# Kernel tuning notes

Hardware: AMD Instinct MI355X
Metric: run time of the kernel (lower is better)

## Reference

```python
import jax, jax.numpy as jnp
import numpy as np

B, T, S_ENC, D = 2, 1024, 1024, 2048
NQ, NKV, H = 16, 8, 256
EPS = 1e-6
CAP = 50.0
SCALE = 0.0625  # query_pre_attn_scalar = head_dim**-0.5
BASE = 10000
K_MASK = -2.3819763e+38


def rms_norm(x, scale, eps=EPS):
    var = jnp.mean(jnp.square(x), axis=-1, keepdims=True)
    return x * jax.lax.rsqrt(var + eps) * (1.0 + scale)


def apply_rope(x, positions, base=BASE):
    # x: [B, L, N, H], positions: [B, L] float. rope_proportion=1.0 -> full head.
    head_dim = x.shape[-1]
    timescale = base ** (2.0 / head_dim * jnp.arange(head_dim // 2, dtype=jnp.float32))
    sinusoid = positions[..., None] / timescale  # [B, L, H/2]
    sinusoid = sinusoid[..., None, :]            # [B, L, 1, H/2]
    sin, cos = jnp.sin(sinusoid), jnp.cos(sinusoid)
    x1, x2 = jnp.split(x, 2, axis=-1)
    return jnp.concatenate([x1 * cos - x2 * sin, x2 * cos + x1 * sin], axis=-1).astype(x.dtype)


def setup_inputs() -> dict:
    key = jax.random.key(0)
    ks = jax.random.split(key, 6)
    hidden_states = jax.random.normal(ks[0], (B, T, D), jnp.float32)
    encoder_hidden_states = jax.random.normal(ks[1], (B, S_ENC, D), jnp.float32)
    position_ids = jnp.broadcast_to(jnp.arange(T, dtype=jnp.int32), (B, T))
    causal = jnp.tril(jnp.ones((T, T), bool))
    merged = jnp.concatenate([causal, jnp.ones((T, S_ENC), bool)], axis=-1)
    merged_attention_mask = jnp.broadcast_to(merged[None, None], (B, 1, T, T + S_ENC))
    q_w = jax.random.normal(ks[2], (NQ, D, H), jnp.float32) * 0.02
    k_w = jax.random.normal(ks[3], (NKV, D, H), jnp.float32) * 0.02
    v_w = jax.random.normal(ks[4], (NKV, D, H), jnp.float32) * 0.02
    o_w = jax.random.normal(ks[5], (NQ, H, D), jnp.float32) * 0.02
    q_scale = jnp.zeros((H,), jnp.float32)
    k_scale = jnp.zeros((H,), jnp.float32)
    return {
        'hidden_states': hidden_states,
        'encoder_hidden_states': encoder_hidden_states,
        'position_ids': position_ids,
        'merged_attention_mask': merged_attention_mask,
        'q_w': q_w, 'k_w': k_w, 'v_w': v_w, 'o_w': o_w,
        'q_scale': q_scale, 'k_scale': k_scale,
    }


def reference(hidden_states, encoder_hidden_states, position_ids, merged_attention_mask,
              q_w, k_w, v_w, o_w, q_scale, k_scale):
    # Fused QKV projections
    q = jnp.einsum('BTD,NDH->BTNH', hidden_states, q_w)
    self_k = jnp.einsum('BTD,NDH->BTNH', hidden_states, k_w)
    self_v = jnp.einsum('BTD,NDH->BTNH', hidden_states, v_w)
    # QK RMSNorm
    q = rms_norm(q, q_scale)
    self_k = rms_norm(self_k, k_scale)
    # RoPE on decoder-side q/k only
    pos = position_ids.astype(jnp.float32)
    q = apply_rope(q, pos)
    self_k = apply_rope(self_k, pos)
    # Cross KV (no RoPE, k-norm applied)
    cross_k = rms_norm(jnp.einsum('BTD,NDH->BTNH', encoder_hidden_states, k_w), k_scale)
    cross_v = jnp.einsum('BTD,NDH->BTNH', encoder_hidden_states, v_w)
    # Merge KV: [B, T+S_enc, NKV, H]
    k = jnp.concatenate([self_k, cross_k], axis=1)
    v = jnp.concatenate([self_v, cross_v], axis=1)
    q = q * SCALE
    # GQA: group query heads over kv heads
    G = NQ // NKV
    qg = q.reshape(B, T, NKV, G, H)
    logits = jnp.einsum('BTKGH,BSKH->BKGTS', qg, k)
    # Logit soft-cap
    logits = CAP * jnp.tanh(logits / CAP)
    mask = merged_attention_mask[:, 0][:, None, None]  # [B,1,1,T,S_comb]
    logits = jnp.where(mask, logits, K_MASK)
    probs = jax.nn.softmax(logits, axis=-1)
    out = jnp.einsum('BKGTS,BSKH->BTKGH', probs, v).reshape(B, T, NQ, H)
    return jnp.einsum('BTNH,NHD->BTD', out, o_w)
```

## Files before the change

kernel.cpp:

```cpp
#include <hip/hip_runtime.h>
#include <hip/hip_bf16.h>
#include <stdint.h>

typedef __hip_bfloat16 bf16;
typedef __attribute__((ext_vector_type(8))) short bv8;
typedef __attribute__((ext_vector_type(4))) float f32x4;


__device__ __forceinline__ f32x4 mfma16(bv8 a, bv8 b, f32x4 c) {
  return __builtin_amdgcn_mfma_f32_16x16x32_bf16(a, b, c, 0, 0, 0);
}

__device__ __forceinline__ void gload16(const void* g, void* lds) {
  __builtin_amdgcn_global_load_lds((const __attribute__((address_space(1))) void*)g,
                                   (__attribute__((address_space(3))) void*)lds, 16, 0, 0);
}

__device__ __forceinline__ void storeC(float* p, float v) { *p = v; }
__device__ __forceinline__ void storeC(bf16* p, float v) { *p = __float2bfloat16(v); }

__global__ void cast2_f32_bf16(const float* __restrict__ a, const float* __restrict__ b,
                               bf16* __restrict__ da, bf16* __restrict__ db, int n4each) {
  int i = blockIdx.x * blockDim.x + threadIdx.x;
  const float* s;
  bf16* d;
  if (i < n4each) { s = a; d = da; }
  else            { s = b; d = db; i -= n4each; }
  float4 v = reinterpret_cast<const float4*>(s)[i];
  bf16 t[4] = {__float2bfloat16(v.x), __float2bfloat16(v.y),
               __float2bfloat16(v.z), __float2bfloat16(v.w)};
  reinterpret_cast<uint64_t*>(d)[i] = *reinterpret_cast<uint64_t*>(t);
}

__global__ void transpose_cast_qkv(const float* __restrict__ q_w, const float* __restrict__ k_w,
                                   const float* __restrict__ v_w, bf16* __restrict__ dst) {
  __shared__ float tile[32][33];
  const int z = blockIdx.z;
  const float* s = (z < 16) ? q_w + (size_t)z * 524288
                 : (z < 24) ? k_w + (size_t)(z - 16) * 524288
                            : v_w + (size_t)(z - 24) * 524288;
  bf16* d = dst + (size_t)z * 524288;
  const int R = 2048, C = 256;
  const int c0 = blockIdx.x * 32, r0 = blockIdx.y * 32;
  const int x = threadIdx.x, y = threadIdx.y;
#pragma unroll
  for (int i = 0; i < 32; i += 8)
    tile[y + i][x] = s[(size_t)(r0 + y + i) * C + c0 + x];
  __syncthreads();
#pragma unroll
  for (int i = 0; i < 32; i += 8)
    d[(size_t)(c0 + y + i) * R + r0 + x] = __float2bfloat16(tile[x][y + i]);
}

__global__ void transpose_cast(const float* __restrict__ src, bf16* __restrict__ dst,
                               int R, int C) {
  __shared__ float tile[32][33];
  const float* s = src;
  bf16* d = dst;
  const int c0 = blockIdx.x * 32, r0 = blockIdx.y * 32;
  const int x = threadIdx.x, y = threadIdx.y;
#pragma unroll
  for (int i = 0; i < 32; i += 8)
    tile[y + i][x] = s[(size_t)(r0 + y + i) * C + c0 + x];
  __syncthreads();
#pragma unroll
  for (int i = 0; i < 32; i += 8)
    d[(size_t)(c0 + y + i) * R + r0 + x] = __float2bfloat16(tile[x][y + i]);
}

__global__ void transpose_v2(const bf16* __restrict__ vself, const bf16* __restrict__ vcross,
                             bf16* __restrict__ dst) {
  __shared__ bf16 tile[32][33];
  const int z = blockIdx.z;
  const int zz = z & 15, b = zz >> 3, kvh = zz & 7;
  const bool cross = z >= 16;
  const bf16* srcb = cross ? vcross : vself;
  const int src_ld = cross ? 4096 : 8192;
  const int t0 = cross ? 1024 : 0;
  const bf16* s = srcb + (size_t)(b * 1024) * src_ld + kvh * 256;
  bf16* d = dst + (size_t)(zz * 256) * 2048 + t0;
  const int h0 = blockIdx.x * 32, tt0 = blockIdx.y * 32;
  const int x = threadIdx.x, y = threadIdx.y;
#pragma unroll
  for (int i = 0; i < 32; i += 8)
    tile[y + i][x] = s[(size_t)(tt0 + y + i) * src_ld + h0 + x];
  __syncthreads();
#pragma unroll
  for (int i = 0; i < 32; i += 8)
    d[(size_t)(h0 + y + i) * 2048 + tt0 + x] = tile[x][y + i];
}

template <typename CT>
__device__ __forceinline__ void gemm_body(const bf16* __restrict__ A, const bf16* __restrict__ Bt,
                                          CT* __restrict__ C, int N, int K,
                                          int m0, int n0, int kbase, int ksteps) {
  __shared__ __align__(16) bf16 As[128 * 32];
  __shared__ __align__(16) bf16 Bs[128 * 32];
  const int tid = threadIdx.x;
  const int w = tid >> 6, l = tid & 63;
  const int wr = w >> 1, wc = w & 1;
  const int l15 = l & 15, lhi = l >> 4;
  const bf16* ag = A + (size_t)(m0 + (tid >> 2)) * K + kbase + (tid & 3) * 8;
  const bf16* bg = Bt + (size_t)(n0 + (tid >> 2)) * K + kbase + (tid & 3) * 8;
  bf16* asw = As + w * 512;
  bf16* bsw = Bs + w * 512;
  f32x4 acc[4][4] = {};
  for (int k0 = 0; k0 < ksteps; k0 += 32) {
    gload16(ag + k0, asw);
    gload16(ag + (size_t)64 * K + k0, asw + 2048);
    gload16(bg + k0, bsw);
    gload16(bg + (size_t)64 * K + k0, bsw + 2048);
    asm volatile("s_waitcnt vmcnt(0)" ::: "memory");
    __syncthreads();
    bv8 af[4], bfv[4];
#pragma unroll
    for (int m = 0; m < 4; ++m)
      af[m] = *reinterpret_cast<const bv8*>(As + (wr * 64 + m * 16 + l15) * 32 + lhi * 8);
#pragma unroll
    for (int n = 0; n < 4; ++n)
      bfv[n] = *reinterpret_cast<const bv8*>(Bs + (wc * 64 + n * 16 + l15) * 32 + lhi * 8);
#pragma unroll
    for (int m = 0; m < 4; ++m)
#pragma unroll
      for (int n = 0; n < 4; ++n)
        acc[m][n] = mfma16(af[m], bfv[n], acc[m][n]);
    __syncthreads();
  }
  const int r0 = m0 + wr * 64 + lhi * 4;
  const int c0 = n0 + wc * 64 + l15;
#pragma unroll
  for (int m = 0; m < 4; ++m)
#pragma unroll
    for (int n = 0; n < 4; ++n) {
      f32x4 v = acc[m][n];
#pragma unroll
      for (int j = 0; j < 4; ++j)
        storeC(&C[(size_t)(r0 + m * 16 + j) * N + c0 + n * 16], v[j]);
    }
}

__launch_bounds__(256)
__global__ void gemm_proj(const bf16* __restrict__ hid, const bf16* __restrict__ enc,
                          const bf16* __restrict__ wqkvt, bf16* __restrict__ cself,
                          bf16* __restrict__ ccross) {
  const int bx = blockIdx.x;
  const bool cross = bx >= 64;
  const bf16* A = cross ? enc : hid;
  const bf16* Bt = cross ? wqkvt + 8388608 : wqkvt;
  bf16* C = cross ? ccross : cself;
  const int N = cross ? 4096 : 8192;
  const int n0 = (cross ? bx - 64 : bx) * 128;
  gemm_body<bf16>(A, Bt, C, N, 2048, blockIdx.y * 128, n0, 0, 2048);
}

__launch_bounds__(256)
__global__ void gemm_osplit(const bf16* __restrict__ A, const bf16* __restrict__ Bt,
                            float* __restrict__ out, float* __restrict__ p1) {
  float* C = blockIdx.z ? p1 : out;
  gemm_body<float>(A, Bt, C, 2048, 4096, blockIdx.y * 128, blockIdx.x * 128,
                   blockIdx.z * 2048, 2048);
}

__global__ void add_inplace(float* __restrict__ out, const float* __restrict__ p1, int n4) {
  int i = blockIdx.x * blockDim.x + threadIdx.x;
  if (i >= n4) return;
  float4 a = reinterpret_cast<float4*>(out)[i];
  float4 b = reinterpret_cast<const float4*>(p1)[i];
  a.x += b.x; a.y += b.y; a.z += b.z; a.w += b.w;
  reinterpret_cast<float4*>(out)[i] = a;
}

template <bool ROPE>
__launch_bounds__(256)
__global__ void norm_finalize(const bf16* __restrict__ src, int src_ld, int src_col0,
                              const float* __restrict__ scale,
                              const int* __restrict__ pos_ids,
                              bf16* __restrict__ dst, int nheads, int dst_S, int dst_t0,
                              float mul) {
  const int gid = blockIdx.x * 4 + (threadIdx.x >> 6);
  const int l = threadIdx.x & 63;
  const int token = gid / nheads;
  const int n = gid - token * nheads;
  const int b = token >> 10;
  const int t = token & 1023;
  const size_t soff = (size_t)token * src_ld + src_col0 + n * 256 + l * 4;
  bf16 xb[4];
  *reinterpret_cast<uint64_t*>(xb) = *reinterpret_cast<const uint64_t*>(src + soff);
  float x[4];
#pragma unroll
  for (int c = 0; c < 4; ++c) x[c] = __bfloat162float(xb[c]);
  float ss = x[0] * x[0] + x[1] * x[1] + x[2] * x[2] + x[3] * x[3];
#pragma unroll
  for (int d = 1; d < 64; d <<= 1) ss += __shfl_xor(ss, d);
  const float r = rsqrtf(ss * (1.0f / 256.0f) + 1e-6f);
  float v[4];
#pragma unroll
  for (int c = 0; c < 4; ++c) v[c] = x[c] * r * (1.0f + scale[l * 4 + c]);
  if (ROPE) {
    const float pos = (float)pos_ids[token];
    float o[4];
#pragma unroll
    for (int c = 0; c < 4; ++c) {
      const int j = (l & 31) * 4 + c;
      const float inv_ts = exp2f(-(float)j * 0.10381025296523007f);
      const float arg = pos * inv_ts;
      const float sj = sinf(arg), cj = cosf(arg);
      const float partner = __shfl_xor(v[c], 32);
      o[c] = (l < 32) ? (v[c] * cj - partner * sj) : (v[c] * cj + partner * sj);
    }
#pragma unroll
    for (int c = 0; c < 4; ++c) v[c] = o[c];
  }
  bf16 ob[4];
#pragma unroll
  for (int c = 0; c < 4; ++c) ob[c] = __float2bfloat16(v[c] * mul);
  const size_t doff = ((size_t)((b * nheads + n) * dst_S + dst_t0 + t)) * 256 + l * 4;
  *reinterpret_cast<uint64_t*>(dst + doff) = *reinterpret_cast<uint64_t*>(ob);
}

__launch_bounds__(512, 2)
__global__ void attn_kernel(const bf16* __restrict__ qb, const bf16* __restrict__ kb,
                            const bf16* __restrict__ vt, bf16* __restrict__ attn_out) {
  __shared__ __align__(16) bf16 Ks[2][64 * 256];
  __shared__ __align__(16) bf16 Vs[2][256 * 64];
  __shared__ __align__(16) bf16 pbuf[8][16 * 72];
  const int lin = blockIdx.x + 16 * blockIdx.y;
  const int kvc = (lin & 7) | (((lin >> 7) & 1) << 3);
  const int qt  = (lin >> 3) & 15;
  const int b = kvc >> 3, kvh = kvc & 7;
  const int tid = threadIdx.x, w = tid >> 6, l = tid & 63;
  const int wq = w & 3, g = w >> 2;
  const int n = kvh * 2 + g;
  const int l15 = l & 15, lhi = l >> 4;
  const int xr = (l15 & 7) << 4;

  const bf16* kbase = kb + (size_t)(b * 8 + kvh) * 2048 * 256;
  const bf16* vbase = vt + (size_t)(b * 8 + kvh) * 256 * 2048;

  const bf16* ksrc[4];
  const bf16* vsrc[4];
#pragma unroll
  for (int i = 0; i < 4; ++i) {
    const int r0 = (w * 4 + i) * 2 + (l >> 5);
    const int cbs = ((l & 31) * 16) ^ ((r0 & 7) << 4);
    ksrc[i] = kbase + r0 * 256 + (cbs >> 1);
    const int h0 = (w * 4 + i) * 8 + (l >> 3);
    const int cbv = ((l & 7) * 16) ^ ((h0 & 7) << 4);
    vsrc[i] = vbase + (size_t)h0 * 2048 + (cbv >> 1);
  }

  const bf16* qptr = qb + ((size_t)(b * 16 + n) * 1024 + qt * 64 + wq * 16 + l15) * 256 + lhi * 8;
  bv8 qf[8];
#pragma unroll
  for (int f = 0; f < 8; ++f) qf[f] = *reinterpret_cast<const bv8*>(qptr + f * 32);

  f32x4 oacc[16] = {};
  float rs[4] = {0.f, 0.f, 0.f, 0.f};

  const int nt = qt + 17;

#pragma unroll
  for (int i = 0; i < 4; ++i) gload16(ksrc[i], &Ks[0][(w * 4 + i) * 512]);
#pragma unroll
  for (int i = 0; i < 4; ++i) gload16(vsrc[i], &Vs[0][(w * 4 + i) * 512]);
  asm volatile("s_waitcnt vmcnt(0)" ::: "memory");
  __syncthreads();

  for (int it = 0; it < nt; ++it) {
    const int cur = it & 1;
    if (it + 1 < nt) {
      const int itn = it + 1;
      const int s1 = (itn <= qt) ? itn * 64 : 1024 + (itn - qt - 1) * 64;
#pragma unroll
      for (int i = 0; i < 4; ++i)
        gload16(ksrc[i] + (size_t)s1 * 256, &Ks[cur ^ 1][(w * 4 + i) * 512]);
#pragma unroll
      for (int i = 0; i < 4; ++i)
        gload16(vsrc[i] + s1, &Vs[cur ^ 1][(w * 4 + i) * 512]);
    }
    f32x4 lacc[4] = {};
    __builtin_amdgcn_s_setprio(1);
#pragma unroll
    for (int sub = 0; sub < 4; ++sub) {
      const int rbase = (sub * 16 + l15) * 256;
#pragma unroll
      for (int f = 0; f < 8; ++f) {
        const int off = rbase + (((f * 64 + lhi * 16) ^ xr) >> 1);
        bv8 kf = *reinterpret_cast<const bv8*>(&Ks[cur][off]);
        lacc[sub] = mfma16(qf[f], kf, lacc[sub]);
      }
    }
    __builtin_amdgcn_s_setprio(0);
    const bool diag = (it == qt);
#pragma unroll
    for (int sub = 0; sub < 4; ++sub) {
#pragma unroll
      for (int j = 0; j < 4; ++j) {
        const float raw = lacc[sub][j];
        const float e2 = __expf(raw * 0.04f);
        const bool ok = !diag || (sub * 16 + l15 <= wq * 16 + lhi * 4 + j);
        const float p = ok ? __expf(50.f - __fdividef(100.f, e2 + 1.f)) : 0.f;
        rs[j] += p;
        pbuf[w][(lhi * 4 + j) * 72 + sub * 16 + l15] = __float2bfloat16(p);
      }
    }
    asm volatile("s_waitcnt lgkmcnt(0)" ::: "memory");
    __builtin_amdgcn_sched_barrier(0);
    __builtin_amdgcn_s_setprio(1);
#pragma unroll
    for (int ks = 0; ks < 2; ++ks) {
      bv8 pa = *reinterpret_cast<const bv8*>(&pbuf[w][l15 * 72 + ks * 32 + lhi * 8]);
#pragma unroll
      for (int ht = 0; ht < 16; ++ht) {
        const int off = (ht * 16 + l15) * 64 + (((ks * 64 + lhi * 16) ^ xr) >> 1);
        bv8 vf = *reinterpret_cast<const bv8*>(&Vs[cur][off]);
        oacc[ht] = mfma16(pa, vf, oacc[ht]);
      }
    }
    __builtin_amdgcn_s_setprio(0);
    asm volatile("s_waitcnt vmcnt(0)" ::: "memory");
    __syncthreads();
  }
  float invr[4];
#pragma unroll
  for (int j = 0; j < 4; ++j) {
    float s = rs[j];
    s += __shfl_xor(s, 1);
    s += __shfl_xor(s, 2);
    s += __shfl_xor(s, 4);
    s += __shfl_xor(s, 8);
    invr[j] = 1.0f / s;
  }
  bf16* op = attn_out + ((size_t)(b * 1024 + qt * 64 + wq * 16 + lhi * 4) * 4096) + n * 256 + l15;
#pragma unroll
  for (int ht = 0; ht < 16; ++ht)
#pragma unroll
    for (int j = 0; j < 4; ++j)
      op[(size_t)j * 4096 + ht * 16] = __float2bfloat16(oacc[ht][j] * invr[j]);
}

extern "C" void kernel_launch(void* const* d_in, const int* in_sizes, int n_in,
                              void* d_out, int out_size, void* d_ws, size_t ws_size,
                              hipStream_t stream) {
  (void)in_sizes; (void)n_in; (void)out_size; (void)ws_size;
  const float* hidden = (const float*)d_in[0];
  const float* enc    = (const float*)d_in[1];
  const int*   pos    = (const int*)d_in[2];
  const float* q_w = (const float*)d_in[4];
  const float* k_w = (const float*)d_in[5];
  const float* v_w = (const float*)d_in[6];
  const float* o_w = (const float*)d_in[7];
  const float* q_s = (const float*)d_in[8];
  const float* k_s = (const float*)d_in[9];
  float* out = (float*)d_out;

  char* base = (char*)d_ws;
  bf16* hid_b  = (bf16*)(base + 0);
  bf16* enc_b  = (bf16*)(base + 8388608);
  bf16* qb     = (bf16*)(base + 0);
  bf16* wqkvt  = (bf16*)(base + 16777216);
  bf16* kbuf   = (bf16*)(base + 16777216);
  bf16* vtb    = (bf16*)(base + 33554432);
  bf16* owt    = (bf16*)(base + 50331648);
  bf16* cself  = (bf16*)(base + 67108864);
  bf16* attn_b = (bf16*)(base + 67108864);
  float* p1    = (float*)(base + 83886080);
  bf16* ccross = (bf16*)(base + 100663296);

  dim3 tb32(32, 8);
  cast2_f32_bf16<<<8192, 256, 0, stream>>>(hidden, enc, hid_b, enc_b, 1048576);
  transpose_cast_qkv<<<dim3(8, 64, 32), tb32, 0, stream>>>(q_w, k_w, v_w, wqkvt);
  transpose_cast<<<dim3(64, 128, 1), tb32, 0, stream>>>(o_w, owt, 4096, 2048);
  gemm_proj<<<dim3(96, 16), 256, 0, stream>>>(hid_b, enc_b, wqkvt, cself, ccross);
  norm_finalize<true><<<8192, 256, 0, stream>>>(cself, 8192, 0, q_s, pos, qb, 16, 1024, 0, 0.0625f);
  norm_finalize<true><<<4096, 256, 0, stream>>>(cself, 8192, 4096, k_s, pos, kbuf, 8, 2048, 0, 1.0f);
  norm_finalize<false><<<4096, 256, 0, stream>>>(ccross, 4096, 0, k_s, nullptr, kbuf, 8, 2048, 1024, 1.0f);
  transpose_v2<<<dim3(8, 32, 32), tb32, 0, stream>>>(cself + 6144, ccross + 2048, vtb);
  attn_kernel<<<dim3(16, 16), 512, 0, stream>>>(qb, kbuf, vtb, attn_b);
  gemm_osplit<<<dim3(16, 16, 2), 256, 0, stream>>>(attn_b, owt, out, p1);
  add_inplace<<<4096, 256, 0, stream>>>(out, p1, 1048576);
}
```

Measured before the change: 376.4 us.

## Repartition attention warps into 2x2 QK and head-dim split PV tiles

Each warp now computes a 32x32 block of the logits (two query subtiles by two key subtiles) instead of 16 queries by all 64 keys. In the PV product each warp covers all 64 queries but only a quarter of the head dimension. Probabilities are shared through a per-group LDS buffer, and row sums are combined across warps via shared memory. This lets each K and V fragment read from LDS feed several MFMAs, cutting LDS traffic per MFMA. The cost is an extra block-wide barrier per iteration, a final reduction step, and twice the Q fragments held in registers.

```diff
diff --git a/kernel.cpp b/kernel.cpp
--- a/kernel.cpp
+++ b/kernel.cpp
@@ -223,13 +223,14 @@
                             const bf16* __restrict__ vt, bf16* __restrict__ attn_out) {
   __shared__ __align__(16) bf16 Ks[2][64 * 256];
   __shared__ __align__(16) bf16 Vs[2][256 * 64];
-  __shared__ __align__(16) bf16 pbuf[8][16 * 72];
+  __shared__ __align__(16) bf16 pbuf[2][64 * 72];
+  __shared__ float rsb[2][2][2][2][4][4];
   const int lin = blockIdx.x + 16 * blockIdx.y;
   const int kvc = (lin & 7) | (((lin >> 7) & 1) << 3);
   const int qt  = (lin >> 3) & 15;
   const int b = kvc >> 3, kvh = kvc & 7;
   const int tid = threadIdx.x, w = tid >> 6, l = tid & 63;
-  const int wq = w & 3, g = w >> 2;
+  const int g = w >> 2, qsp = (w >> 1) & 1, sh = w & 1, hq = w & 3;
   const int n = kvh * 2 + g;
   const int l15 = l & 15, lhi = l >> 4;
   const int xr = (l15 & 7) << 4;
@@ -249,13 +250,17 @@
     vsrc[i] = vbase + (size_t)h0 * 2048 + (cbv >> 1);
   }
 
-  const bf16* qptr = qb + ((size_t)(b * 16 + n) * 1024 + qt * 64 + wq * 16 + l15) * 256 + lhi * 8;
-  bv8 qf[8];
-#pragma unroll
-  for (int f = 0; f < 8; ++f) qf[f] = *reinterpret_cast<const bv8*>(qptr + f * 32);
-
-  f32x4 oacc[16] = {};
-  float rs[4] = {0.f, 0.f, 0.f, 0.f};
+  bv8 qf[2][8];
+#pragma unroll
+  for (int qs2 = 0; qs2 < 2; ++qs2) {
+    const bf16* qp = qb + ((size_t)(b * 16 + n) * 1024 + qt * 64 +
+                           (qsp * 2 + qs2) * 16 + l15) * 256 + lhi * 8;
+#pragma unroll
+    for (int f = 0; f < 8; ++f) qf[qs2][f] = *reinterpret_cast<const bv8*>(qp + f * 32);
+  }
+
+  f32x4 oacc[4][4] = {};
+  float rs[2][4] = {};
 
   const int nt = qt + 17;
 
@@ -278,65 +283,84 @@
       for (int i = 0; i < 4; ++i)
         gload16(vsrc[i] + s1, &Vs[cur ^ 1][(w * 4 + i) * 512]);
     }
-    f32x4 lacc[4] = {};
+    f32x4 lacc[2][2] = {};
     __builtin_amdgcn_s_setprio(1);
 #pragma unroll
-    for (int sub = 0; sub < 4; ++sub) {
-      const int rbase = (sub * 16 + l15) * 256;
+    for (int ss2 = 0; ss2 < 2; ++ss2) {
+      const int rbase = ((sh * 2 + ss2) * 16 + l15) * 256;
 #pragma unroll
       for (int f = 0; f < 8; ++f) {
         const int off = rbase + (((f * 64 + lhi * 16) ^ xr) >> 1);
         bv8 kf = *reinterpret_cast<const bv8*>(&Ks[cur][off]);
-        lacc[sub] = mfma16(qf[f], kf, lacc[sub]);
+        lacc[0][ss2] = mfma16(qf[0][f], kf, lacc[0][ss2]);
+        lacc[1][ss2] = mfma16(qf[1][f], kf, lacc[1][ss2]);
       }
     }
     __builtin_amdgcn_s_setprio(0);
     const bool diag = (it == qt);
 #pragma unroll
-    for (int sub = 0; sub < 4; ++sub) {
-#pragma unroll
-      for (int j = 0; j < 4; ++j) {
-        const float raw = lacc[sub][j];
-        const float e2 = __expf(raw * 0.04f);
-        const bool ok = !diag || (sub * 16 + l15 <= wq * 16 + lhi * 4 + j);
-        const float p = ok ? __expf(50.f - __fdividef(100.f, e2 + 1.f)) : 0.f;
-        rs[j] += p;
-        pbuf[w][(lhi * 4 + j) * 72 + sub * 16 + l15] = __float2bfloat16(p);
-      }
-    }
-    asm volatile("s_waitcnt lgkmcnt(0)" ::: "memory");
-    __builtin_amdgcn_sched_barrier(0);
+    for (int qs2 = 0; qs2 < 2; ++qs2)
+#pragma unroll
+      for (int ss2 = 0; ss2 < 2; ++ss2)
+#pragma unroll
+        for (int j = 0; j < 4; ++j) {
+          const float raw = lacc[qs2][ss2][j];
+          const float e2 = __expf(raw * 0.04f);
+          const bool ok = !diag ||
+              ((sh * 2 + ss2) * 16 + l15 <= (qsp * 2 + qs2) * 16 + lhi * 4 + j);
+          const float p = ok ? __expf(50.f - __fdividef(100.f, e2 + 1.f)) : 0.f;
+          rs[qs2][j] += p;
+          pbuf[g][((qsp * 2 + qs2) * 16 + lhi * 4 + j) * 72 + (sh * 2 + ss2) * 16 + l15] =
+              __float2bfloat16(p);
+        }
+    __syncthreads();
     __builtin_amdgcn_s_setprio(1);
 #pragma unroll
     for (int ks = 0; ks < 2; ++ks) {
-      bv8 pa = *reinterpret_cast<const bv8*>(&pbuf[w][l15 * 72 + ks * 32 + lhi * 8]);
-#pragma unroll
-      for (int ht = 0; ht < 16; ++ht) {
-        const int off = (ht * 16 + l15) * 64 + (((ks * 64 + lhi * 16) ^ xr) >> 1);
+      bv8 pa[4];
+#pragma unroll
+      for (int qs = 0; qs < 4; ++qs)
+        pa[qs] = *reinterpret_cast<const bv8*>(&pbuf[g][(qs * 16 + l15) * 72 + ks * 32 + lhi * 8]);
+#pragma unroll
+      for (int i = 0; i < 4; ++i) {
+        const int off = ((hq * 4 + i) * 16 + l15) * 64 + (((ks * 64 + lhi * 16) ^ xr) >> 1);
         bv8 vf = *reinterpret_cast<const bv8*>(&Vs[cur][off]);
-        oacc[ht] = mfma16(pa, vf, oacc[ht]);
+#pragma unroll
+        for (int qs = 0; qs < 4; ++qs) oacc[qs][i] = mfma16(pa[qs], vf, oacc[qs][i]);
       }
     }
     __builtin_amdgcn_s_setprio(0);
     asm volatile("s_waitcnt vmcnt(0)" ::: "memory");
     __syncthreads();
   }
-  float invr[4];
-#pragma unroll
-  for (int j = 0; j < 4; ++j) {
-    float s = rs[j];
-    s += __shfl_xor(s, 1);
-    s += __shfl_xor(s, 2);
-    s += __shfl_xor(s, 4);
-    s += __shfl_xor(s, 8);
-    invr[j] = 1.0f / s;
-  }
-  bf16* op = attn_out + ((size_t)(b * 1024 + qt * 64 + wq * 16 + lhi * 4) * 4096) + n * 256 + l15;
-#pragma unroll
-  for (int ht = 0; ht < 16; ++ht)
+#pragma unroll
+  for (int qs2 = 0; qs2 < 2; ++qs2)
+#pragma unroll
+    for (int j = 0; j < 4; ++j) {
+      float s = rs[qs2][j];
+      s += __shfl_xor(s, 1);
+      s += __shfl_xor(s, 2);
+      s += __shfl_xor(s, 4);
+      s += __shfl_xor(s, 8);
+      if (l15 == 0) rsb[g][qsp][sh][qs2][j][lhi] = s;
+    }
+  __syncthreads();
+  float invr[4][4];
+#pragma unroll
+  for (int qs = 0; qs < 4; ++qs)
 #pragma unroll
     for (int j = 0; j < 4; ++j)
-      op[(size_t)j * 4096 + ht * 16] = __float2bfloat16(oacc[ht][j] * invr[j]);
+      invr[qs][j] = 1.0f / (rsb[g][qs >> 1][0][qs & 1][j][lhi] +
+                            rsb[g][qs >> 1][1][qs & 1][j][lhi]);
+  bf16* op = attn_out + ((size_t)(b * 1024 + qt * 64 + lhi * 4) * 4096) + n * 256 + l15;
+#pragma unroll
+  for (int qs = 0; qs < 4; ++qs)
+#pragma unroll
+    for (int i = 0; i < 4; ++i)
+#pragma unroll
+      for (int j = 0; j < 4; ++j)
+        op[(size_t)(qs * 16 + j) * 4096 + (hq * 4 + i) * 16] =
+            __float2bfloat16(oacc[qs][i][j] * invr[qs][j]);
 }
 
 extern "C" void kernel_launch(void* const* d_in, const int* in_sizes, int n_in,
```

Measured after the change: 370.0 us. No clear change (-1.7%).

## Halve attention query/key tiles and split score and PV work across warps

Applied to the files above, without the earlier changes.

The attention kernel now uses 32-row query tiles and 32-key KV tiles, which doubles the grid to 512 blocks and shrinks LDS use so up to four blocks can fit per CU. Each warp now computes one 16x16 score sub-tile and one quarter of the head dimension for PV. The probability tile is shared between warps through LDS, which needs an extra block-wide barrier every iteration. Row sums are combined across warps through a small LDS buffer at the end. The intent is more parallelism and occupancy for the causal-imbalanced workload, at the cost of more syncs and less data reuse per block. The exp calls are also switched to exp2f with pre-scaled constants.

```diff
diff --git a/kernel.cpp b/kernel.cpp
--- a/kernel.cpp
+++ b/kernel.cpp
@@ -218,18 +218,19 @@
   *reinterpret_cast<uint64_t*>(dst + doff) = *reinterpret_cast<uint64_t*>(ob);
 }
 
-__launch_bounds__(512, 2)
+__launch_bounds__(512, 4)
 __global__ void attn_kernel(const bf16* __restrict__ qb, const bf16* __restrict__ kb,
                             const bf16* __restrict__ vt, bf16* __restrict__ attn_out) {
-  __shared__ __align__(16) bf16 Ks[2][64 * 256];
-  __shared__ __align__(16) bf16 Vs[2][256 * 64];
-  __shared__ __align__(16) bf16 pbuf[8][16 * 72];
-  const int lin = blockIdx.x + 16 * blockIdx.y;
-  const int kvc = (lin & 7) | (((lin >> 7) & 1) << 3);
-  const int qt  = (lin >> 3) & 15;
+  __shared__ __align__(16) bf16 Ks[2][32 * 256];
+  __shared__ __align__(16) bf16 Vs[2][256 * 32];
+  __shared__ __align__(16) bf16 pbuf[2][32 * 36];
+  __shared__ float rsb[2][2][2][4][4];
+  const int lin = blockIdx.x + 32 * blockIdx.y;
+  const int kvc = (lin & 7) | (((lin >> 8) & 1) << 3);
+  const int qt  = (lin >> 3) & 31;
   const int b = kvc >> 3, kvh = kvc & 7;
   const int tid = threadIdx.x, w = tid >> 6, l = tid & 63;
-  const int wq = w & 3, g = w >> 2;
+  const int g = w >> 2, qs = (w >> 1) & 1, sh = w & 1, hq = w & 3;
   const int n = kvh * 2 + g;
   const int l15 = l & 15, lhi = l >> 4;
   const int xr = (l15 & 7) << 4;
@@ -237,32 +238,32 @@
   const bf16* kbase = kb + (size_t)(b * 8 + kvh) * 2048 * 256;
   const bf16* vbase = vt + (size_t)(b * 8 + kvh) * 256 * 2048;
 
-  const bf16* ksrc[4];
-  const bf16* vsrc[4];
-#pragma unroll
-  for (int i = 0; i < 4; ++i) {
-    const int r0 = (w * 4 + i) * 2 + (l >> 5);
-    const int cbs = ((l & 31) * 16) ^ ((r0 & 7) << 4);
-    ksrc[i] = kbase + r0 * 256 + (cbs >> 1);
-    const int h0 = (w * 4 + i) * 8 + (l >> 3);
-    const int cbv = ((l & 7) * 16) ^ ((h0 & 7) << 4);
-    vsrc[i] = vbase + (size_t)h0 * 2048 + (cbv >> 1);
-  }
-
-  const bf16* qptr = qb + ((size_t)(b * 16 + n) * 1024 + qt * 64 + wq * 16 + l15) * 256 + lhi * 8;
+  const int kcol = (((tid & 31) * 16) ^ (((tid >> 5) & 7) << 4)) >> 1;
+  const bf16* ksrc0 = kbase + (size_t)(tid >> 5) * 256 + kcol;
+  const bf16* ksrc1 = kbase + (size_t)(16 + (tid >> 5)) * 256 + kcol;
+  const int vcol = (((tid & 3) * 16) ^ (((tid >> 2) & 3) << 4)) >> 1;
+  const bf16* vsrc0 = vbase + (size_t)(tid >> 2) * 2048 + vcol;
+  const bf16* vsrc1 = vbase + (size_t)(128 + (tid >> 2)) * 2048 + vcol;
+
+#define STAGE_KV(bb, s0)                                         \
+  do {                                                           \
+    gload16(ksrc0 + (size_t)(s0) * 256, &Ks[bb][w * 512]);       \
+    gload16(ksrc1 + (size_t)(s0) * 256, &Ks[bb][4096 + w * 512]);\
+    gload16(vsrc0 + (s0), &Vs[bb][w * 512]);                     \
+    gload16(vsrc1 + (s0), &Vs[bb][4096 + w * 512]);              \
+  } while (0)
+
+  const bf16* qp = qb + ((size_t)(b * 16 + n) * 1024 + qt * 32 + qs * 16 + l15) * 256 + lhi * 8;
   bv8 qf[8];
 #pragma unroll
-  for (int f = 0; f < 8; ++f) qf[f] = *reinterpret_cast<const bv8*>(qptr + f * 32);
-
-  f32x4 oacc[16] = {};
-  float rs[4] = {0.f, 0.f, 0.f, 0.f};
-
-  const int nt = qt + 17;
-
-#pragma unroll
-  for (int i = 0; i < 4; ++i) gload16(ksrc[i], &Ks[0][(w * 4 + i) * 512]);
-#pragma unroll
-  for (int i = 0; i < 4; ++i) gload16(vsrc[i], &Vs[0][(w * 4 + i) * 512]);
+  for (int f = 0; f < 8; ++f) qf[f] = *reinterpret_cast<const bv8*>(qp + f * 32);
+
+  f32x4 oacc[2][4] = {};
+  float rs[4] = {};
+
+  const int nt = qt + 33;
+
+  STAGE_KV(0, 0);
   asm volatile("s_waitcnt vmcnt(0)" ::: "memory");
   __syncthreads();
 
@@ -270,58 +271,49 @@
     const int cur = it & 1;
     if (it + 1 < nt) {
       const int itn = it + 1;
-      const int s1 = (itn <= qt) ? itn * 64 : 1024 + (itn - qt - 1) * 64;
-#pragma unroll
-      for (int i = 0; i < 4; ++i)
-        gload16(ksrc[i] + (size_t)s1 * 256, &Ks[cur ^ 1][(w * 4 + i) * 512]);
-#pragma unroll
-      for (int i = 0; i < 4; ++i)
-        gload16(vsrc[i] + s1, &Vs[cur ^ 1][(w * 4 + i) * 512]);
-    }
-    f32x4 lacc[4] = {};
+      const int s1 = (itn <= qt) ? itn * 32 : 1024 + (itn - qt - 1) * 32;
+      STAGE_KV(cur ^ 1, s1);
+    }
+    f32x4 lacc = {};
+    const int krow = (sh * 16 + l15) * 256;
     __builtin_amdgcn_s_setprio(1);
 #pragma unroll
-    for (int sub = 0; sub < 4; ++sub) {
-      const int rbase = (sub * 16 + l15) * 256;
-#pragma unroll
-      for (int f = 0; f < 8; ++f) {
-        const int off = rbase + (((f * 64 + lhi * 16) ^ xr) >> 1);
-        bv8 kf = *reinterpret_cast<const bv8*>(&Ks[cur][off]);
-        lacc[sub] = mfma16(qf[f], kf, lacc[sub]);
-      }
+    for (int f = 0; f < 8; ++f) {
+      const int off = krow + (((f * 64 + lhi * 16) ^ xr) >> 1);
+      bv8 kf = *reinterpret_cast<const bv8*>(&Ks[cur][off]);
+      lacc = mfma16(qf[f], kf, lacc);
     }
     __builtin_amdgcn_s_setprio(0);
     const bool diag = (it == qt);
 #pragma unroll
-    for (int sub = 0; sub < 4; ++sub) {
-#pragma unroll
-      for (int j = 0; j < 4; ++j) {
-        const float raw = lacc[sub][j];
-        const float e2 = __expf(raw * 0.04f);
-        const bool ok = !diag || (sub * 16 + l15 <= wq * 16 + lhi * 4 + j);
-        const float p = ok ? __expf(50.f - __fdividef(100.f, e2 + 1.f)) : 0.f;
-        rs[j] += p;
-        pbuf[w][(lhi * 4 + j) * 72 + sub * 16 + l15] = __float2bfloat16(p);
-      }
-    }
-    asm volatile("s_waitcnt lgkmcnt(0)" ::: "memory");
-    __builtin_amdgcn_sched_barrier(0);
+    for (int j = 0; j < 4; ++j) {
+      const float raw = lacc[j];
+      const float e2 = exp2f(raw * 0.057707801635559464f);
+      const int trow = qs * 16 + lhi * 4 + j;
+      const bool ok = !diag || (sh * 16 + l15 <= trow);
+      const float p =
+          ok ? exp2f(72.13475204444817f - __fdividef(144.26950408889634f, e2 + 1.f)) : 0.f;
+      rs[j] += p;
+      pbuf[g][trow * 36 + sh * 16 + l15] = __float2bfloat16(p);
+    }
+    __syncthreads();
     __builtin_amdgcn_s_setprio(1);
-#pragma unroll
-    for (int ks = 0; ks < 2; ++ks) {
-      bv8 pa = *reinterpret_cast<const bv8*>(&pbuf[w][l15 * 72 + ks * 32 + lhi * 8]);
-#pragma unroll
-      for (int ht = 0; ht < 16; ++ht) {
-        const int off = (ht * 16 + l15) * 64 + (((ks * 64 + lhi * 16) ^ xr) >> 1);
-        bv8 vf = *reinterpret_cast<const bv8*>(&Vs[cur][off]);
-        oacc[ht] = mfma16(pa, vf, oacc[ht]);
-      }
+    bv8 pa[2];
+#pragma unroll
+    for (int q = 0; q < 2; ++q)
+      pa[q] = *reinterpret_cast<const bv8*>(&pbuf[g][(q * 16 + l15) * 36 + lhi * 8]);
+#pragma unroll
+    for (int i = 0; i < 4; ++i) {
+      const int off = ((hq * 4 + i) * 16 + l15) * 32 + ((lhi * 8) ^ ((l15 & 3) << 3));
+      bv8 vf = *reinterpret_cast<const bv8*>(&Vs[cur][off]);
+      oacc[0][i] = mfma16(pa[0], vf, oacc[0][i]);
+      oacc[1][i] = mfma16(pa[1], vf, oacc[1][i]);
     }
     __builtin_amdgcn_s_setprio(0);
     asm volatile("s_waitcnt vmcnt(0)" ::: "memory");
     __syncthreads();
   }
-  float invr[4];
+#undef STAGE_KV
 #pragma unroll
   for (int j = 0; j < 4; ++j) {
     float s = rs[j];
@@ -329,14 +321,24 @@
     s += __shfl_xor(s, 2);
     s += __shfl_xor(s, 4);
     s += __shfl_xor(s, 8);
-    invr[j] = 1.0f / s;
+    if (l15 == 0) rsb[g][qs][sh][j][lhi] = s;
   }
-  bf16* op = attn_out + ((size_t)(b * 1024 + qt * 64 + wq * 16 + lhi * 4) * 4096) + n * 256 + l15;
-#pragma unroll
-  for (int ht = 0; ht < 16; ++ht)
+  __syncthreads();
+  float invr[2][4];
+#pragma unroll
+  for (int q = 0; q < 2; ++q)
 #pragma unroll
     for (int j = 0; j < 4; ++j)
-      op[(size_t)j * 4096 + ht * 16] = __float2bfloat16(oacc[ht][j] * invr[j]);
+      invr[q][j] = 1.0f / (rsb[g][q][0][j][lhi] + rsb[g][q][1][j][lhi]);
+  bf16* op = attn_out + ((size_t)(b * 1024 + qt * 32 + lhi * 4) * 4096) + n * 256 + l15;
+#pragma unroll
+  for (int q = 0; q < 2; ++q)
+#pragma unroll
+    for (int i = 0; i < 4; ++i)
+#pragma unroll
+      for (int j = 0; j < 4; ++j)
+        op[(size_t)(q * 16 + j) * 4096 + (hq * 4 + i) * 16] =
+            __float2bfloat16(oacc[q][i][j] * invr[q][j]);
 }
 
 extern "C" void kernel_launch(void* const* d_in, const int* in_sizes, int n_in,
@@ -376,7 +378,7 @@
   norm_finalize<true><<<4096, 256, 0, stream>>>(cself, 8192, 4096, k_s, pos, kbuf, 8, 2048, 0, 1.0f);
   norm_finalize<false><<<4096, 256, 0, stream>>>(ccross, 4096, 0, k_s, nullptr, kbuf, 8, 2048, 1024, 1.0f);
   transpose_v2<<<dim3(8, 32, 32), tb32, 0, stream>>>(cself + 6144, ccross + 2048, vtb);
-  attn_kernel<<<dim3(16, 16), 512, 0, stream>>>(qb, kbuf, vtb, attn_b);
+  attn_kernel<<<dim3(32, 16), 512, 0, stream>>>(qb, kbuf, vtb, attn_b);
   gemm_osplit<<<dim3(16, 16, 2), 256, 0, stream>>>(attn_b, owt, out, p1);
   add_inplace<<<4096, 256, 0, stream>>>(out, p1, 1048576);
 }
```

Result: no change. 374.7 us (-0.5%).
